# Kernel optimization log

Measured on AMD Instinct MI355X. Metric: run time of the kernel, lower is better.

The kernel has to match this reference:

```python
import jax, jax.numpy as jnp
import numpy as np

GRAVITY = 9.81
W_INERTIA = 1.0
W_GRAVITY = 0.01
W_STRAIN = 1.0

V = 500_000
E = 2_000_000


def setup_inputs() -> dict:
    key = jax.random.key(0)
    ks = jax.random.split(key, 7)
    pos_next = jax.random.normal(ks[0], (V, 3), dtype=jnp.float32)
    pos_curr = jax.random.normal(ks[1], (V, 3), dtype=jnp.float32)
    pos_prev = jax.random.normal(ks[2], (V, 3), dtype=jnp.float32)
    mass = jax.random.uniform(ks[3], (V, 1), dtype=jnp.float32)
    elements = jax.random.randint(ks[4], (E, 4), 0, V, dtype=jnp.int64)
    rest_volumes = jax.random.uniform(ks[5], (E,), dtype=jnp.float32)
    rest_inv = jax.random.normal(ks[6], (E, 3, 3), dtype=jnp.float32)
    lam = jnp.float32(1.0)
    mu = jnpp_one = jnp.float32(1.0)
    return {
        "pos_next": pos_next, "pos_curr": pos_curr, "pos_prev": pos_prev,
        "mass": mass, "elements": elements, "rest_volumes": rest_volumes,
        "rest_inv": rest_inv, "lam": lam, "mu": mu,
    }


def _det3(F):
    # F: (E, 3, 3)
    return (F[:, 0, 0] * (F[:, 1, 1] * F[:, 2, 2] - F[:, 1, 2] * F[:, 2, 1])
            - F[:, 0, 1] * (F[:, 1, 0] * F[:, 2, 2] - F[:, 1, 2] * F[:, 2, 0])
            + F[:, 0, 2] * (F[:, 1, 0] * F[:, 2, 1] - F[:, 1, 1] * F[:, 2, 0]))


def _physics_loss(pos_next, pos_curr, pos_prev, mass, elements, rest_volumes, rest_inv, lam, mu):
    # Inertia: mean over all V*3 entries of 0.5 * m * a^2
    accel = pos_next + pos_prev - 2.0 * pos_curr          # (V, 3)
    inertia = 0.5 * jnp.mean(mass * accel * accel)
    # Gravity: -mean(m * g * y)
    gravity = -jnp.mean(mass * GRAVITY * pos_curr[:, 1:2])
    # Strain (Neo-Hookean) on pos_next
    v = pos_next[elements]                                 # (E, 4, 3)
    Ds = jnp.stack([v[:, 1] - v[:, 0], v[:, 2] - v[:, 0], v[:, 3] - v[:, 0]], axis=-1)  # (E,3,3)
    F_def = jnp.einsum('eij,ejk->eik', Ds, rest_inv)       # (E, 3, 3)
    det_F = jnp.maximum(_det3(F_def), 1e-8)
    log_det = jnp.log(det_F)
    tr_FtF = jnp.sum(F_def * F_def, axis=(1, 2))           # trace(F^T F) = ||F||_F^2
    psi = 0.5 * lam * log_det ** 2 - mu * log_det + 0.5 * mu * (tr_FtF - 3.0)
    strain = jnp.mean(psi * rest_volumes)
    return W_INERTIA * inertia + W_GRAVITY * gravity + W_STRAIN * strain


def reference(pos_next, pos_curr, pos_prev, mass, elements, rest_volumes, rest_inv, lam, mu):
    return _physics_loss(pos_next, pos_curr, pos_prev, mass, elements, rest_volumes, rest_inv, lam, mu)
```

## Files before the change

kernel.cpp:

```cpp
#include <hip/hip_runtime.h>

#define GRAVITY_F 9.81f
#define EPT 4

typedef int   v4i __attribute__((ext_vector_type(4)));
typedef float v4f __attribute__((ext_vector_type(4), aligned(16)));

__device__ __forceinline__ float blockReduceSum(float val) {
    #pragma unroll
    for (int off = 32; off > 0; off >>= 1)
        val += __shfl_down(val, off, 64);
    __shared__ float smem[16];
    const int lane = threadIdx.x & 63;
    const int wave = threadIdx.x >> 6;
    if (lane == 0) smem[wave] = val;
    __syncthreads();
    const int nwaves = (blockDim.x + 63) >> 6;
    val = 0.0f;
    if (wave == 0) {
        if (lane < nwaves) val = smem[lane];
        #pragma unroll
        for (int off = 8; off > 0; off >>= 1)
            val += __shfl_down(val, off, 64);
    }
    return val;
}

__global__ void __launch_bounds__(256, 3)
fused_kernel(const float* __restrict__ pn,
             const float* __restrict__ pc,
             const float* __restrict__ pp,
             const float* __restrict__ mass,
             const int*   __restrict__ elems,
             const float* __restrict__ vols,
             const float* __restrict__ rinv,
             const float* __restrict__ lam_p,
             const float* __restrict__ mu_p,
             float* __restrict__ partials,
             int V, int E, int Eblocks,
             float sI, float sG, float sS) {
    float local = 0.0f;

    if ((int)blockIdx.x < Eblocks) {
        const float lam = lam_p[0];
        const float mu  = mu_p[0];
        const int t  = blockIdx.x * 256 + threadIdx.x;
        const int e0 = t * 4;

        float rf[36];
        v4i   idx[EPT];
        float vol[EPT];
        float sc[EPT];

        if (e0 + EPT <= E) {
            v4f rq[9];
            const v4f* Rp = (const v4f*)(rinv + 36 * (size_t)t);
            #pragma unroll
            for (int k = 0; k < 9; ++k)
                rq[k] = __builtin_nontemporal_load(Rp + k);
            const v4f vv = __builtin_nontemporal_load((const v4f*)(vols + 4 * (size_t)t));
            #pragma unroll
            for (int i = 0; i < EPT; ++i)
                idx[i] = __builtin_nontemporal_load((const v4i*)elems + (4 * (size_t)t + i));
            #pragma unroll
            for (int k = 0; k < 9; ++k)
                #pragma unroll
                for (int j = 0; j < 4; ++j)
                    rf[4 * k + j] = rq[k][j];
            #pragma unroll
            for (int i = 0; i < EPT; ++i) { vol[i] = vv[i]; sc[i] = sS; }
        } else {
            #pragma unroll
            for (int i = 0; i < EPT; ++i) {
                const int e  = e0 + i;
                const int ec = e < E ? e : (E - 1);
                sc[i]  = e < E ? sS : 0.0f;
                vol[i] = __builtin_nontemporal_load(vols + ec);
                idx[i] = __builtin_nontemporal_load((const v4i*)elems + ec);
                #pragma unroll
                for (int k = 0; k < 9; ++k)
                    rf[9 * i + k] = __builtin_nontemporal_load(rinv + 9 * (size_t)ec + k);
            }
        }

        float x[EPT][4][3];
        #pragma unroll
        for (int i = 0; i < EPT; ++i) {
            const float* p0 = pn + 3 * (size_t)idx[i].x;
            const float* p1 = pn + 3 * (size_t)idx[i].y;
            const float* p2 = pn + 3 * (size_t)idx[i].z;
            const float* p3 = pn + 3 * (size_t)idx[i].w;
            #pragma unroll
            for (int r = 0; r < 3; ++r) {
                x[i][0][r] = p0[r];
                x[i][1][r] = p1[r];
                x[i][2][r] = p2[r];
                x[i][3][r] = p3[r];
            }
        }

        asm volatile("" ::
            "v"(x[0][0][0]), "v"(x[0][0][1]), "v"(x[0][0][2]),
            "v"(x[0][1][0]), "v"(x[0][1][1]), "v"(x[0][1][2]),
            "v"(x[0][2][0]), "v"(x[0][2][1]), "v"(x[0][2][2]),
            "v"(x[0][3][0]), "v"(x[0][3][1]), "v"(x[0][3][2]),
            "v"(x[1][0][0]), "v"(x[1][0][1]), "v"(x[1][0][2]),
            "v"(x[1][1][0]), "v"(x[1][1][1]), "v"(x[1][1][2]),
            "v"(x[1][2][0]), "v"(x[1][2][1]), "v"(x[1][2][2]),
            "v"(x[1][3][0]), "v"(x[1][3][1]), "v"(x[1][3][2]));
        asm volatile("" ::
            "v"(x[2][0][0]), "v"(x[2][0][1]), "v"(x[2][0][2]),
            "v"(x[2][1][0]), "v"(x[2][1][1]), "v"(x[2][1][2]),
            "v"(x[2][2][0]), "v"(x[2][2][1]), "v"(x[2][2][2]),
            "v"(x[2][3][0]), "v"(x[2][3][1]), "v"(x[2][3][2]),
            "v"(x[3][0][0]), "v"(x[3][0][1]), "v"(x[3][0][2]),
            "v"(x[3][1][0]), "v"(x[3][1][1]), "v"(x[3][1][2]),
            "v"(x[3][2][0]), "v"(x[3][2][1]), "v"(x[3][2][2]),
            "v"(x[3][3][0]), "v"(x[3][3][1]), "v"(x[3][3][2]));
        asm volatile("" ::
            "v"(rf[0]),  "v"(rf[1]),  "v"(rf[2]),  "v"(rf[3]),  "v"(rf[4]),
            "v"(rf[5]),  "v"(rf[6]),  "v"(rf[7]),  "v"(rf[8]),  "v"(rf[9]),
            "v"(rf[10]), "v"(rf[11]), "v"(rf[12]), "v"(rf[13]), "v"(rf[14]),
            "v"(rf[15]), "v"(rf[16]), "v"(rf[17]));
        asm volatile("" ::
            "v"(rf[18]), "v"(rf[19]), "v"(rf[20]), "v"(rf[21]), "v"(rf[22]),
            "v"(rf[23]), "v"(rf[24]), "v"(rf[25]), "v"(rf[26]), "v"(rf[27]),
            "v"(rf[28]), "v"(rf[29]), "v"(rf[30]), "v"(rf[31]), "v"(rf[32]),
            "v"(rf[33]), "v"(rf[34]), "v"(rf[35]),
            "v"(vol[0]), "v"(vol[1]), "v"(vol[2]), "v"(vol[3]));

        #pragma unroll
        for (int i = 0; i < EPT; ++i) {
            float d[3][3];
            #pragma unroll
            for (int r = 0; r < 3; ++r) {
                d[r][0] = x[i][1][r] - x[i][0][r];
                d[r][1] = x[i][2][r] - x[i][0][r];
                d[r][2] = x[i][3][r] - x[i][0][r];
            }
            float F[3][3];
            #pragma unroll
            for (int r = 0; r < 3; ++r)
                #pragma unroll
                for (int k = 0; k < 3; ++k)
                    F[r][k] = d[r][0] * rf[9 * i + 0 + k]
                            + d[r][1] * rf[9 * i + 3 + k]
                            + d[r][2] * rf[9 * i + 6 + k];
            const float det = F[0][0] * (F[1][1] * F[2][2] - F[1][2] * F[2][1])
                            - F[0][1] * (F[1][0] * F[2][2] - F[1][2] * F[2][0])
                            + F[0][2] * (F[1][0] * F[2][1] - F[1][1] * F[2][0]);
            const float ld = logf(fmaxf(det, 1e-8f));
            float tr = 0.0f;
            #pragma unroll
            for (int r = 0; r < 3; ++r)
                #pragma unroll
                for (int k = 0; k < 3; ++k)
                    tr += F[r][k] * F[r][k];
            const float psi = 0.5f * lam * ld * ld - mu * ld + 0.5f * mu * (tr - 3.0f);
            local += sc[i] * (psi * vol[i]);
        }
    } else {
        const int g  = (blockIdx.x - Eblocks) * blockDim.x + threadIdx.x;
        const int v0 = g * 4;
        if (v0 + 4 <= V) {
            const v4f m4 = *(const v4f*)(mass + v0);
            const v4f n0 = *(const v4f*)(pn + 3 * v0);
            const v4f n1 = *(const v4f*)(pn + 3 * v0 + 4);
            const v4f n2 = *(const v4f*)(pn + 3 * v0 + 8);
            const v4f c0 = __builtin_nontemporal_load((const v4f*)(pc + 3 * v0));
            const v4f c1 = __builtin_nontemporal_load((const v4f*)(pc + 3 * v0 + 4));
            const v4f c2 = __builtin_nontemporal_load((const v4f*)(pc + 3 * v0 + 8));
            const v4f q0 = __builtin_nontemporal_load((const v4f*)(pp + 3 * v0));
            const v4f q1 = __builtin_nontemporal_load((const v4f*)(pp + 3 * v0 + 4));
            const v4f q2 = __builtin_nontemporal_load((const v4f*)(pp + 3 * v0 + 8));
            const v4f N[3] = { n0, n1, n2 };
            const v4f C[3] = { c0, c1, c2 };
            const v4f Q[3] = { q0, q1, q2 };
            #pragma unroll
            for (int i = 0; i < 4; ++i) {
                float acc = 0.0f;
                #pragma unroll
                for (int r = 0; r < 3; ++r) {
                    const int k = 3 * i + r;
                    const float a = N[k >> 2][k & 3] + Q[k >> 2][k & 3]
                                  - 2.0f * C[k >> 2][k & 3];
                    acc += a * a;
                }
                const int ky = 3 * i + 1;
                const float y = C[ky >> 2][ky & 3];
                local += sI * (m4[i] * acc) + sG * (m4[i] * y);
            }
        } else {
            for (int v = v0; v < V; ++v) {
                const float m  = mass[v];
                const float p0 = pc[3 * v + 0];
                const float y  = pc[3 * v + 1];
                const float p2 = pc[3 * v + 2];
                const float a0 = pn[3 * v + 0] + pp[3 * v + 0] - 2.0f * p0;
                const float a1 = pn[3 * v + 1] + pp[3 * v + 1] - 2.0f * y;
                const float a2 = pn[3 * v + 2] + pp[3 * v + 2] - 2.0f * p2;
                local += sI * (m * (a0 * a0 + a1 * a1 + a2 * a2)) + sG * (m * y);
            }
        }
    }

    const float tot = blockReduceSum(local);
    if (threadIdx.x == 0) partials[blockIdx.x] = tot;
}

__global__ void reduce_kernel(const float* __restrict__ partials, int n,
                              float* __restrict__ out) {
    double s = 0.0;
    for (int i = threadIdx.x; i < n; i += blockDim.x)
        s += (double)partials[i];
    __shared__ double sm[256];
    sm[threadIdx.x] = s;
    __syncthreads();
    #pragma unroll
    for (int off = 128; off > 0; off >>= 1) {
        if (threadIdx.x < off) sm[threadIdx.x] += sm[threadIdx.x + off];
        __syncthreads();
    }
    if (threadIdx.x == 0) out[0] = (float)sm[0];
}

extern "C" void kernel_launch(void* const* d_in, const int* in_sizes, int n_in,
                              void* d_out, int out_size, void* d_ws, size_t ws_size,
                              hipStream_t stream) {
    const float* pos_next = (const float*)d_in[0];
    const float* pos_curr = (const float*)d_in[1];
    const float* pos_prev = (const float*)d_in[2];
    const float* mass     = (const float*)d_in[3];
    const int*   elements = (const int*)d_in[4];
    const float* rest_vol = (const float*)d_in[5];
    const float* rest_inv = (const float*)d_in[6];
    const float* lam_p    = (const float*)d_in[7];
    const float* mu_p     = (const float*)d_in[8];
    float* out = (float*)d_out;

    const int V = in_sizes[3];
    const int E = in_sizes[5];

    const float sI = 0.5f / (3.0f * (float)V);
    const float sG = -0.01f * GRAVITY_F / (float)V;
    const float sS = 1.0f / (float)E;

    const int block = 256;
    const int Eblocks  = (E + EPT * block - 1) / (EPT * block);
    const int Vgroups  = (V + 3) / 4;
    const int Vblocks4 = (Vgroups + block - 1) / block;
    const int grid = Eblocks + Vblocks4;

    float* partials = (float*)d_ws;

    fused_kernel<<<grid, block, 0, stream>>>(pos_next, pos_curr, pos_prev,
                                             mass, elements, rest_vol,
                                             rest_inv, lam_p, mu_p,
                                             partials, V, E, Eblocks,
                                             sI, sG, sS);
    reduce_kernel<<<1, 256, 0, stream>>>(partials, grid, out);
}
```

Measured before the change: 238.0 us.

## Pack vertex positions to fp16 table and gather compressed in element kernel

Splits the fused kernel into a vertex kernel, which also packs pos_next into an 8-byte fp16 table in a global device array, and a separate element kernel. The element kernel gathers the packed table instead of 12-byte fp32 vertices, which cuts random-gather traffic. When the fp16-derived determinant is small it recomputes that element from the fp32 positions. This adds an extra kernel launch with a dependency between the two kernels, plus the cost of writing the table. It also introduces fp16 precision error in the Frobenius trace term, which the fallback does not guard.

```diff
diff --git a/kernel.cpp b/kernel.cpp
--- a/kernel.cpp
+++ b/kernel.cpp
@@ -1,10 +1,13 @@
 #include <hip/hip_runtime.h>
+#include <hip/hip_fp16.h>
 
 #define GRAVITY_F 9.81f
-#define EPT 4
+#define TAB_CAP_V 520000
 
 typedef int   v4i __attribute__((ext_vector_type(4)));
 typedef float v4f __attribute__((ext_vector_type(4), aligned(16)));
+
+__device__ __align__(16) uint2 g_tab[TAB_CAP_V + 2];
 
 __device__ __forceinline__ float blockReduceSum(float val) {
     #pragma unroll
@@ -26,97 +29,166 @@
     return val;
 }
 
-__global__ void __launch_bounds__(256, 3)
-fused_kernel(const float* __restrict__ pn,
-             const float* __restrict__ pc,
-             const float* __restrict__ pp,
-             const float* __restrict__ mass,
-             const int*   __restrict__ elems,
-             const float* __restrict__ vols,
-             const float* __restrict__ rinv,
-             const float* __restrict__ lam_p,
-             const float* __restrict__ mu_p,
-             float* __restrict__ partials,
-             int V, int E, int Eblocks,
-             float sI, float sG, float sS) {
+__device__ __forceinline__ uint2 packVert(float x, float y, float z) {
+    uint2 w;
+    w.x = (unsigned)__half_as_ushort(__float2half(x))
+        | ((unsigned)__half_as_ushort(__float2half(y)) << 16);
+    w.y = (unsigned)__half_as_ushort(__float2half(z));
+    return w;
+}
+
+__device__ __forceinline__ void dec3(uint2 w, float* o) {
+    o[0] = __half2float(__ushort_as_half((unsigned short)(w.x & 0xffffu)));
+    o[1] = __half2float(__ushort_as_half((unsigned short)(w.x >> 16)));
+    o[2] = __half2float(__ushort_as_half((unsigned short)(w.y & 0xffffu)));
+}
+
+__global__ void __launch_bounds__(256)
+pack_vert_kernel(const float* __restrict__ pn,
+                 const float* __restrict__ pc,
+                 const float* __restrict__ pp,
+                 const float* __restrict__ mass,
+                 float* __restrict__ partials,
+                 int V, int doPack, float sI, float sG) {
+    const int g  = blockIdx.x * blockDim.x + threadIdx.x;
+    const int v0 = g * 4;
     float local = 0.0f;
 
-    if ((int)blockIdx.x < Eblocks) {
-        const float lam = lam_p[0];
-        const float mu  = mu_p[0];
-        const int t  = blockIdx.x * 256 + threadIdx.x;
-        const int e0 = t * 4;
-
-        float rf[36];
-        v4i   idx[EPT];
-        float vol[EPT];
-        float sc[EPT];
-
-        if (e0 + EPT <= E) {
-            v4f rq[9];
-            const v4f* Rp = (const v4f*)(rinv + 36 * (size_t)t);
+    if (v0 + 4 <= V) {
+        const v4f m4 = *(const v4f*)(mass + v0);
+        const v4f n0 = *(const v4f*)(pn + 3 * v0);
+        const v4f n1 = *(const v4f*)(pn + 3 * v0 + 4);
+        const v4f n2 = *(const v4f*)(pn + 3 * v0 + 8);
+        const v4f c0 = __builtin_nontemporal_load((const v4f*)(pc + 3 * v0));
+        const v4f c1 = __builtin_nontemporal_load((const v4f*)(pc + 3 * v0 + 4));
+        const v4f c2 = __builtin_nontemporal_load((const v4f*)(pc + 3 * v0 + 8));
+        const v4f q0 = __builtin_nontemporal_load((const v4f*)(pp + 3 * v0));
+        const v4f q1 = __builtin_nontemporal_load((const v4f*)(pp + 3 * v0 + 4));
+        const v4f q2 = __builtin_nontemporal_load((const v4f*)(pp + 3 * v0 + 8));
+        const v4f N[3] = { n0, n1, n2 };
+        const v4f C[3] = { c0, c1, c2 };
+        const v4f Q[3] = { q0, q1, q2 };
+
+        if (doPack) {
+            uint2 w[4];
+            #pragma unroll
+            for (int i = 0; i < 4; ++i) {
+                const int k = 3 * i;
+                w[i] = packVert(N[(k + 0) >> 2][(k + 0) & 3],
+                                N[(k + 1) >> 2][(k + 1) & 3],
+                                N[(k + 2) >> 2][(k + 2) & 3]);
+            }
+            uint4* dst = reinterpret_cast<uint4*>(&g_tab[v0]);
+            dst[0] = make_uint4(w[0].x, w[0].y, w[1].x, w[1].y);
+            dst[1] = make_uint4(w[2].x, w[2].y, w[3].x, w[3].y);
+        }
+
+        #pragma unroll
+        for (int i = 0; i < 4; ++i) {
+            float acc = 0.0f;
+            #pragma unroll
+            for (int r = 0; r < 3; ++r) {
+                const int k = 3 * i + r;
+                const float a = N[k >> 2][k & 3] + Q[k >> 2][k & 3]
+                              - 2.0f * C[k >> 2][k & 3];
+                acc += a * a;
+            }
+            const int ky = 3 * i + 1;
+            const float y = C[ky >> 2][ky & 3];
+            local += sI * (m4[i] * acc) + sG * (m4[i] * y);
+        }
+    } else {
+        for (int v = v0; v < V; ++v) {
+            const float m  = mass[v];
+            const float x0 = pn[3 * v + 0];
+            const float x1 = pn[3 * v + 1];
+            const float x2 = pn[3 * v + 2];
+            if (doPack) g_tab[v] = packVert(x0, x1, x2);
+            const float p0 = pc[3 * v + 0];
+            const float y  = pc[3 * v + 1];
+            const float p2 = pc[3 * v + 2];
+            const float a0 = x0 + pp[3 * v + 0] - 2.0f * p0;
+            const float a1 = x1 + pp[3 * v + 1] - 2.0f * y;
+            const float a2 = x2 + pp[3 * v + 2] - 2.0f * p2;
+            local += sI * (m * (a0 * a0 + a1 * a1 + a2 * a2)) + sG * (m * y);
+        }
+    }
+
+    const float tot = blockReduceSum(local);
+    if (threadIdx.x == 0) partials[blockIdx.x] = tot;
+}
+
+template <bool PACKED>
+__global__ void __launch_bounds__(256, 4)
+elem_kernel(const float* __restrict__ pn,
+            const int*   __restrict__ elems,
+            const float* __restrict__ vols,
+            const float* __restrict__ rinv,
+            const float* __restrict__ lam_p,
+            const float* __restrict__ mu_p,
+            float* __restrict__ partials,
+            int E, float sS) {
+    const float lam = lam_p[0];
+    const float mu  = mu_p[0];
+    float local = 0.0f;
+
+    const int t  = blockIdx.x * 256 + threadIdx.x;
+    const int e0 = 4 * t;
+
+    float rf[36];
+    v4i   idx[4];
+    float vol[4];
+    float sc[4];
+
+    if (e0 + 4 <= E) {
+        v4f rq[9];
+        const v4f* Rp = (const v4f*)(rinv + 36 * (size_t)t);
+        #pragma unroll
+        for (int k = 0; k < 9; ++k)
+            rq[k] = __builtin_nontemporal_load(Rp + k);
+        const v4f vv = __builtin_nontemporal_load((const v4f*)(vols + 4 * (size_t)t));
+        #pragma unroll
+        for (int i = 0; i < 4; ++i)
+            idx[i] = __builtin_nontemporal_load((const v4i*)elems + (4 * (size_t)t + i));
+        #pragma unroll
+        for (int k = 0; k < 9; ++k)
+            #pragma unroll
+            for (int j = 0; j < 4; ++j)
+                rf[4 * k + j] = rq[k][j];
+        #pragma unroll
+        for (int i = 0; i < 4; ++i) { vol[i] = vv[i]; sc[i] = sS; }
+    } else {
+        #pragma unroll
+        for (int i = 0; i < 4; ++i) {
+            const int e  = e0 + i;
+            const int ec = e < E ? e : (E - 1);
+            sc[i]  = e < E ? sS : 0.0f;
+            vol[i] = __builtin_nontemporal_load(vols + ec);
+            idx[i] = __builtin_nontemporal_load((const v4i*)elems + ec);
             #pragma unroll
             for (int k = 0; k < 9; ++k)
-                rq[k] = __builtin_nontemporal_load(Rp + k);
-            const v4f vv = __builtin_nontemporal_load((const v4f*)(vols + 4 * (size_t)t));
-            #pragma unroll
-            for (int i = 0; i < EPT; ++i)
-                idx[i] = __builtin_nontemporal_load((const v4i*)elems + (4 * (size_t)t + i));
-            #pragma unroll
-            for (int k = 0; k < 9; ++k)
-                #pragma unroll
-                for (int j = 0; j < 4; ++j)
-                    rf[4 * k + j] = rq[k][j];
-            #pragma unroll
-            for (int i = 0; i < EPT; ++i) { vol[i] = vv[i]; sc[i] = sS; }
-        } else {
-            #pragma unroll
-            for (int i = 0; i < EPT; ++i) {
-                const int e  = e0 + i;
-                const int ec = e < E ? e : (E - 1);
-                sc[i]  = e < E ? sS : 0.0f;
-                vol[i] = __builtin_nontemporal_load(vols + ec);
-                idx[i] = __builtin_nontemporal_load((const v4i*)elems + ec);
-                #pragma unroll
-                for (int k = 0; k < 9; ++k)
-                    rf[9 * i + k] = __builtin_nontemporal_load(rinv + 9 * (size_t)ec + k);
-            }
-        }
-
-        float x[EPT][4][3];
-        #pragma unroll
-        for (int i = 0; i < EPT; ++i) {
-            const float* p0 = pn + 3 * (size_t)idx[i].x;
-            const float* p1 = pn + 3 * (size_t)idx[i].y;
-            const float* p2 = pn + 3 * (size_t)idx[i].z;
-            const float* p3 = pn + 3 * (size_t)idx[i].w;
-            #pragma unroll
-            for (int r = 0; r < 3; ++r) {
-                x[i][0][r] = p0[r];
-                x[i][1][r] = p1[r];
-                x[i][2][r] = p2[r];
-                x[i][3][r] = p3[r];
-            }
-        }
+                rf[9 * i + k] = __builtin_nontemporal_load(rinv + 9 * (size_t)ec + k);
+        }
+    }
+
+    if (PACKED) {
+        uint2 gq[4][4];
+        #pragma unroll
+        for (int i = 0; i < 4; ++i)
+            #pragma unroll
+            for (int j = 0; j < 4; ++j)
+                gq[i][j] = g_tab[(unsigned)idx[i][j]];
 
         asm volatile("" ::
-            "v"(x[0][0][0]), "v"(x[0][0][1]), "v"(x[0][0][2]),
-            "v"(x[0][1][0]), "v"(x[0][1][1]), "v"(x[0][1][2]),
-            "v"(x[0][2][0]), "v"(x[0][2][1]), "v"(x[0][2][2]),
-            "v"(x[0][3][0]), "v"(x[0][3][1]), "v"(x[0][3][2]),
-            "v"(x[1][0][0]), "v"(x[1][0][1]), "v"(x[1][0][2]),
-            "v"(x[1][1][0]), "v"(x[1][1][1]), "v"(x[1][1][2]),
-            "v"(x[1][2][0]), "v"(x[1][2][1]), "v"(x[1][2][2]),
-            "v"(x[1][3][0]), "v"(x[1][3][1]), "v"(x[1][3][2]));
+            "v"(gq[0][0].x), "v"(gq[0][0].y), "v"(gq[0][1].x), "v"(gq[0][1].y),
+            "v"(gq[0][2].x), "v"(gq[0][2].y), "v"(gq[0][3].x), "v"(gq[0][3].y),
+            "v"(gq[1][0].x), "v"(gq[1][0].y), "v"(gq[1][1].x), "v"(gq[1][1].y),
+            "v"(gq[1][2].x), "v"(gq[1][2].y), "v"(gq[1][3].x), "v"(gq[1][3].y));
         asm volatile("" ::
-            "v"(x[2][0][0]), "v"(x[2][0][1]), "v"(x[2][0][2]),
-            "v"(x[2][1][0]), "v"(x[2][1][1]), "v"(x[2][1][2]),
-            "v"(x[2][2][0]), "v"(x[2][2][1]), "v"(x[2][2][2]),
-            "v"(x[2][3][0]), "v"(x[2][3][1]), "v"(x[2][3][2]),
-            "v"(x[3][0][0]), "v"(x[3][0][1]), "v"(x[3][0][2]),
-            "v"(x[3][1][0]), "v"(x[3][1][1]), "v"(x[3][1][2]),
-            "v"(x[3][2][0]), "v"(x[3][2][1]), "v"(x[3][2][2]),
-            "v"(x[3][3][0]), "v"(x[3][3][1]), "v"(x[3][3][2]));
+            "v"(gq[2][0].x), "v"(gq[2][0].y), "v"(gq[2][1].x), "v"(gq[2][1].y),
+            "v"(gq[2][2].x), "v"(gq[2][2].y), "v"(gq[2][3].x), "v"(gq[2][3].y),
+            "v"(gq[3][0].x), "v"(gq[3][0].y), "v"(gq[3][1].x), "v"(gq[3][1].y),
+            "v"(gq[3][2].x), "v"(gq[3][2].y), "v"(gq[3][3].x), "v"(gq[3][3].y));
         asm volatile("" ::
             "v"(rf[0]),  "v"(rf[1]),  "v"(rf[2]),  "v"(rf[3]),  "v"(rf[4]),
             "v"(rf[5]),  "v"(rf[6]),  "v"(rf[7]),  "v"(rf[8]),  "v"(rf[9]),
@@ -130,15 +202,88 @@
             "v"(vol[0]), "v"(vol[1]), "v"(vol[2]), "v"(vol[3]));
 
         #pragma unroll
-        for (int i = 0; i < EPT; ++i) {
-            float d[3][3];
+        for (int i = 0; i < 4; ++i) {
+            float x[4][3];
+            #pragma unroll
+            for (int j = 0; j < 4; ++j)
+                dec3(gq[i][j], x[j]);
+
+            float d[3][3], F[3][3];
             #pragma unroll
             for (int r = 0; r < 3; ++r) {
-                d[r][0] = x[i][1][r] - x[i][0][r];
-                d[r][1] = x[i][2][r] - x[i][0][r];
-                d[r][2] = x[i][3][r] - x[i][0][r];
-            }
-            float F[3][3];
+                d[r][0] = x[1][r] - x[0][r];
+                d[r][1] = x[2][r] - x[0][r];
+                d[r][2] = x[3][r] - x[0][r];
+            }
+            #pragma unroll
+            for (int r = 0; r < 3; ++r)
+                #pragma unroll
+                for (int k = 0; k < 3; ++k)
+                    F[r][k] = d[r][0] * rf[9 * i + 0 + k]
+                            + d[r][1] * rf[9 * i + 3 + k]
+                            + d[r][2] * rf[9 * i + 6 + k];
+            float det = F[0][0] * (F[1][1] * F[2][2] - F[1][2] * F[2][1])
+                      - F[0][1] * (F[1][0] * F[2][2] - F[1][2] * F[2][0])
+                      + F[0][2] * (F[1][0] * F[2][1] - F[1][1] * F[2][0]);
+
+            if (fabsf(det) < 0.5f) {
+                const float* p0 = pn + 3 * (size_t)idx[i].x;
+                const float* p1 = pn + 3 * (size_t)idx[i].y;
+                const float* p2 = pn + 3 * (size_t)idx[i].z;
+                const float* p3 = pn + 3 * (size_t)idx[i].w;
+                #pragma unroll
+                for (int r = 0; r < 3; ++r) {
+                    x[0][r] = p0[r]; x[1][r] = p1[r];
+                    x[2][r] = p2[r]; x[3][r] = p3[r];
+                }
+                #pragma unroll
+                for (int r = 0; r < 3; ++r) {
+                    d[r][0] = x[1][r] - x[0][r];
+                    d[r][1] = x[2][r] - x[0][r];
+                    d[r][2] = x[3][r] - x[0][r];
+                }
+                #pragma unroll
+                for (int r = 0; r < 3; ++r)
+                    #pragma unroll
+                    for (int k = 0; k < 3; ++k)
+                        F[r][k] = d[r][0] * rf[9 * i + 0 + k]
+                                + d[r][1] * rf[9 * i + 3 + k]
+                                + d[r][2] * rf[9 * i + 6 + k];
+                det = F[0][0] * (F[1][1] * F[2][2] - F[1][2] * F[2][1])
+                    - F[0][1] * (F[1][0] * F[2][2] - F[1][2] * F[2][0])
+                    + F[0][2] * (F[1][0] * F[2][1] - F[1][1] * F[2][0]);
+            }
+
+            const float ld = logf(fmaxf(det, 1e-8f));
+            float tr = 0.0f;
+            #pragma unroll
+            for (int r = 0; r < 3; ++r)
+                #pragma unroll
+                for (int k = 0; k < 3; ++k)
+                    tr += F[r][k] * F[r][k];
+            const float psi = 0.5f * lam * ld * ld - mu * ld + 0.5f * mu * (tr - 3.0f);
+            local += sc[i] * (psi * vol[i]);
+        }
+    } else {
+        #pragma unroll
+        for (int i = 0; i < 4; ++i) {
+            float x[4][3];
+            const float* p0 = pn + 3 * (size_t)idx[i].x;
+            const float* p1 = pn + 3 * (size_t)idx[i].y;
+            const float* p2 = pn + 3 * (size_t)idx[i].z;
+            const float* p3 = pn + 3 * (size_t)idx[i].w;
+            #pragma unroll
+            for (int r = 0; r < 3; ++r) {
+                x[0][r] = p0[r]; x[1][r] = p1[r];
+                x[2][r] = p2[r]; x[3][r] = p3[r];
+            }
+            float d[3][3], F[3][3];
+            #pragma unroll
+            for (int r = 0; r < 3; ++r) {
+                d[r][0] = x[1][r] - x[0][r];
+                d[r][1] = x[2][r] - x[0][r];
+                d[r][2] = x[3][r] - x[0][r];
+            }
             #pragma unroll
             for (int r = 0; r < 3; ++r)
                 #pragma unroll
@@ -158,49 +303,6 @@
                     tr += F[r][k] * F[r][k];
             const float psi = 0.5f * lam * ld * ld - mu * ld + 0.5f * mu * (tr - 3.0f);
             local += sc[i] * (psi * vol[i]);
-        }
-    } else {
-        const int g  = (blockIdx.x - Eblocks) * blockDim.x + threadIdx.x;
-        const int v0 = g * 4;
-        if (v0 + 4 <= V) {
-            const v4f m4 = *(const v4f*)(mass + v0);
-            const v4f n0 = *(const v4f*)(pn + 3 * v0);
-            const v4f n1 = *(const v4f*)(pn + 3 * v0 + 4);
-            const v4f n2 = *(const v4f*)(pn + 3 * v0 + 8);
-            const v4f c0 = __builtin_nontemporal_load((const v4f*)(pc + 3 * v0));
-            const v4f c1 = __builtin_nontemporal_load((const v4f*)(pc + 3 * v0 + 4));
-            const v4f c2 = __builtin_nontemporal_load((const v4f*)(pc + 3 * v0 + 8));
-            const v4f q0 = __builtin_nontemporal_load((const v4f*)(pp + 3 * v0));
-            const v4f q1 = __builtin_nontemporal_load((const v4f*)(pp + 3 * v0 + 4));
-            const v4f q2 = __builtin_nontemporal_load((const v4f*)(pp + 3 * v0 + 8));
-            const v4f N[3] = { n0, n1, n2 };
-            const v4f C[3] = { c0, c1, c2 };
-            const v4f Q[3] = { q0, q1, q2 };
-            #pragma unroll
-            for (int i = 0; i < 4; ++i) {
-                float acc = 0.0f;
-                #pragma unroll
-                for (int r = 0; r < 3; ++r) {
-                    const int k = 3 * i + r;
-                    const float a = N[k >> 2][k & 3] + Q[k >> 2][k & 3]
-                                  - 2.0f * C[k >> 2][k & 3];
-                    acc += a * a;
-                }
-                const int ky = 3 * i + 1;
-                const float y = C[ky >> 2][ky & 3];
-                local += sI * (m4[i] * acc) + sG * (m4[i] * y);
-            }
-        } else {
-            for (int v = v0; v < V; ++v) {
-                const float m  = mass[v];
-                const float p0 = pc[3 * v + 0];
-                const float y  = pc[3 * v + 1];
-                const float p2 = pc[3 * v + 2];
-                const float a0 = pn[3 * v + 0] + pp[3 * v + 0] - 2.0f * p0;
-                const float a1 = pn[3 * v + 1] + pp[3 * v + 1] - 2.0f * y;
-                const float a2 = pn[3 * v + 2] + pp[3 * v + 2] - 2.0f * p2;
-                local += sI * (m * (a0 * a0 + a1 * a1 + a2 * a2)) + sG * (m * y);
-            }
         }
     }
 
@@ -246,17 +348,23 @@
     const float sS = 1.0f / (float)E;
 
     const int block = 256;
-    const int Eblocks  = (E + EPT * block - 1) / (EPT * block);
-    const int Vgroups  = (V + 3) / 4;
-    const int Vblocks4 = (Vgroups + block - 1) / block;
-    const int grid = Eblocks + Vblocks4;
+    const int gridV = (((V + 3) / 4) + block - 1) / block;
+    const int gridE = (((E + 3) / 4) + block - 1) / block;
+    const int grid  = gridV + gridE;
+    const int doPack = (V <= TAB_CAP_V) ? 1 : 0;
 
     float* partials = (float*)d_ws;
 
-    fused_kernel<<<grid, block, 0, stream>>>(pos_next, pos_curr, pos_prev,
-                                             mass, elements, rest_vol,
-                                             rest_inv, lam_p, mu_p,
-                                             partials, V, E, Eblocks,
-                                             sI, sG, sS);
+    pack_vert_kernel<<<gridV, block, 0, stream>>>(pos_next, pos_curr, pos_prev,
+                                                  mass, partials, V, doPack, sI, sG);
+    if (doPack) {
+        elem_kernel<true><<<gridE, block, 0, stream>>>(pos_next, elements, rest_vol,
+                                                       rest_inv, lam_p, mu_p,
+                                                       partials + gridV, E, sS);
+    } else {
+        elem_kernel<false><<<gridE, block, 0, stream>>>(pos_next, elements, rest_vol,
+                                                        rest_inv, lam_p, mu_p,
+                                                        partials + gridV, E, sS);
+    }
     reduce_kernel<<<1, 256, 0, stream>>>(partials, grid, out);
 }
```

New measurement: 260.5 us. +9.4%, slower.
